# Kernel optimization log

Hardware: AMD Instinct MI355X
Metric: run time of the kernel (lower is better)

## Reference

```python
import jax, jax.numpy as jnp
import numpy as np

P = 16            # patch_size
D = 256           # hidden_dim == P*P (required by final reshape)
H = 8             # num_heads
HD = D // H       # head_dim


def _sinusoid(n, d):
    # standard sinusoidal positional encoding, interleaved sin/cos
    pos = jnp.arange(n, dtype=jnp.float32)[:, None]            # (n,1)
    i = jnp.arange(0, d, 2, dtype=jnp.float32)                 # (d/2,)
    div = jnp.exp(-i * (jnp.log(10000.0) / d))                 # (d/2,)
    ang = pos * div                                            # (n, d/2)
    return jnp.stack([jnp.sin(ang), jnp.cos(ang)], axis=-1).reshape(n, d)


def _patch_embed(x, w, b):
    # Conv2d(in_ch, D, kernel=P, stride=P) then flatten to (B, N, D)
    e = jax.lax.conv_general_dilated(
        x, w, window_strides=(P, P), padding='VALID',
        dimension_numbers=('NCHW', 'OIHW', 'NCHW'))
    e = e + b[None, :, None, None]
    B = e.shape[0]
    e = e.reshape(B, D, -1).transpose(0, 2, 1)                 # (B, N, D)
    e = e + _sinusoid(e.shape[1], D)[None]                     # positional enc
    return e.reshape(B, -1, H, HD).transpose(0, 2, 1, 3)       # (B, H, N, HD)


def setup_inputs() -> dict:
    key = jax.random.key(0)
    ks = jax.random.split(key, 12)
    B = 16
    inp = {
        'q': jax.random.normal(ks[0], (B, 3, 512, 512), jnp.float32),
        'k': jax.random.normal(ks[1], (B, 3, 512, 512), jnp.float32),
        'v': jax.random.normal(ks[2], (B, 3, 512, 512), jnp.float32),
        'a': jax.random.normal(ks[3], (B, 3, 256, 256), jnp.float32),
    }
    s = 0.02
    for idx, name in enumerate('qkva'):
        inp['w' + name] = jax.random.normal(ks[4 + 2 * idx], (D, 3, P, P), jnp.float32) * s
        inp['b' + name] = jnp.zeros((D,), jnp.float32)
    return inp


def reference(q, k, v, a, wq, bq, wk, bk, wv, bv, wa, ba):
    qh = _patch_embed(q, wq, bq)   # (B,H,Nq,HD), Nq=1024
    kh = _patch_embed(k, wk, bk)   # (B,H,Nk,HD)
    vh = _patch_embed(v, wv, bv)   # (B,H,Nk,HD)
    ah = _patch_embed(a, wa, ba)   # (B,H,Na,HD), Na=256
    scale = HD ** -0.5
    # agent attention: two small softmax matmuls then Q @ (K @ V)
    Qs = jax.nn.softmax(jnp.einsum('bhnd,bhmd->bhnm', qh, ah) * scale, axis=-1)  # (B,H,Nq,Na)
    Ks = jax.nn.softmax(jnp.einsum('bhmd,bhnd->bhmn', ah, kh) * scale, axis=-1)  # (B,H,Na,Nk)
    KV = jnp.einsum('bhmn,bhnd->bhmd', Ks, vh)                                   # (B,H,Na,HD)
    A = jnp.einsum('bhnm,bhmd->bhnd', Qs, KV)                                    # (B,H,Nq,HD)
    B = A.shape[0]
    attn = A.transpose(0, 2, 1, 3).reshape(B, -1, D)            # (B, Nq, D)
    N = attn.shape[1]
    g = int(N ** 0.5)                                           # grid side (32)
    HW = g * P                                                  # 512
    attn = attn.reshape(B, N, P, P)
    attn = attn.reshape(B, g, g, P, P).transpose(0, 1, 3, 2, 4).reshape(B, HW, HW)
    return attn
```

## Files before the change

kernel.cpp:

```cpp
#include <hip/hip_runtime.h>
#include <cstdint>
#include <cstddef>

typedef __bf16 bf16x8 __attribute__((ext_vector_type(8)));
typedef __bf16 bf16x4 __attribute__((ext_vector_type(4)));
typedef float f32x4 __attribute__((ext_vector_type(4)));
typedef unsigned short u16x4 __attribute__((ext_vector_type(4)));
typedef unsigned short u16x8 __attribute__((ext_vector_type(8)));

#define MFMA16(a, b, c) __builtin_amdgcn_mfma_f32_16x16x32_bf16(a, b, c, 0, 0, 0)

__device__ __forceinline__ unsigned short f2bf(float f) {
    unsigned u = __builtin_bit_cast(unsigned, f);
    u = (u + 0x7FFFu + ((u >> 16) & 1u)) >> 16;
    return (unsigned short)u;
}

__global__ __launch_bounds__(256)
void prep(float* __restrict__ pe, float* __restrict__ peT, unsigned short* __restrict__ Wb,
          const float* __restrict__ w0, const float* __restrict__ w1,
          const float* __restrict__ w2, const float* __restrict__ w3) {
    const int bx = blockIdx.x, t = threadIdx.x;
    const float LC = 0.03597789207808881f;
    if (bx < 1024) {
        int n = bx, d = t;
        float div = expf(-(float)(2 * (d >> 1)) * LC);
        float ang = (float)n * div;
        pe[n * 256 + d] = (d & 1) ? cosf(ang) : sinf(ang);
    } else if (bx < 1280) {
        int d = bx - 1024;
        float div = expf(-(float)(2 * (d >> 1)) * LC);
        f32x4 o;
        int n0 = t * 4;
#pragma unroll
        for (int e = 0; e < 4; ++e) {
            float ang = (float)(n0 + e) * div;
            o[e] = (d & 1) ? cosf(ang) : sinf(ang);
        }
        *(f32x4*)&peT[(size_t)d * 1024 + n0] = o;
    } else {
        int i = bx - 1280;
        int tensor = i / 192, blk = i - tensor * 192;
        const float* w = (tensor == 0) ? w0 : (tensor == 1) ? w1 : (tensor == 2) ? w2 : w3;
        int idx4 = blk * 256 + t;
        int d = idx4 / 192;
        int kq = (idx4 - d * 192) * 4;
        f32x4 v = *(const f32x4*)(w + (size_t)idx4 * 4);
        u16x4 o;
#pragma unroll
        for (int e = 0; e < 4; ++e) o[e] = f2bf(v[e]);
        unsigned short* dst = Wb + (size_t)tensor * 196608
                            + (d >> 4) * 12288 + (kq >> 5) * 512
                            + (d & 15) * 32 + (kq & 31);
        *(u16x4*)dst = o;
    }
}

struct EArgs {
    const float* src;
    const unsigned short* Wb;
    const float* bias;
    const float* pe;
    const float* peT;
    unsigned short* dst;
    int Np, lgNp, lgG, S, trans;
};

typedef unsigned short AsTile[128][40];

template<bool TR>
__device__ __forceinline__ void embed_body(const EArgs& A, int m0, int nh, AsTile* As) {
    const int t = threadIdx.x, lane = t & 63, wid = t >> 6;
    const int l15 = lane & 15, l4 = lane >> 4;
    const int wr = wid >> 1, wc = wid & 1;
    const int S = A.S;

    const int sp = t & 127;
    const int sh = t >> 7;
    {
    }
    int p_s = m0 + sp;
    int b_s = p_s >> A.lgNp, n_s = p_s & (A.Np - 1);
    int gy_s = n_s >> A.lgG, gx_s = n_s & ((1 << A.lgG) - 1);
    const float* sbase = A.src + ((size_t)(b_s * 3) * S + gy_s * 16 + sh) * (size_t)S + gx_s * 16;

    auto loadA = [&](int kt, f32x4* g) {
        const float* a = sbase + ((size_t)(kt >> 3) * S + ((kt & 7) << 1)) * (size_t)S;
        g[0] = *(const f32x4*)(a);
        g[1] = *(const f32x4*)(a + 4);
        g[2] = *(const f32x4*)(a + 8);
        g[3] = *(const f32x4*)(a + 12);
    };
    auto writeA = [&](int buf, const f32x4* g) {
        u16x8 o0, o1;
#pragma unroll
        for (int e = 0; e < 4; ++e) {
            o0[e] = f2bf(g[0][e]); o0[4 + e] = f2bf(g[1][e]);
            o1[e] = f2bf(g[2][e]); o1[4 + e] = f2bf(g[3][e]);
        }
        *(u16x8*)&As[buf][sp][sh * 16] = o0;
        *(u16x8*)&As[buf][sp][sh * 16 + 8] = o1;
    };

    const unsigned short* wbase = A.Wb + (size_t)(nh * 8 + wc * 4) * 12288 + l15 * 32 + l4 * 8;
    auto loadW = [&](int kt, bf16x8* wf) {
#pragma unroll
        for (int j = 0; j < 4; ++j) {
            u16x8 r = *(const u16x8*)(wbase + j * 12288 + kt * 512);
            wf[j] = __builtin_bit_cast(bf16x8, r);
        }
    };

    f32x4 acc[4][4];
#pragma unroll
    for (int i = 0; i < 4; ++i)
#pragma unroll
        for (int j = 0; j < 4; ++j) acc[i][j] = f32x4{0.f, 0.f, 0.f, 0.f};

    f32x4 gaA[4], gaB[4];
    bf16x8 wfc[4];
    loadA(0, gaA);
    writeA(0, gaA);
    loadA(1, gaA);
    loadW(0, wfc);
    __syncthreads();

#pragma unroll 2
    for (int kt = 0; kt < 24; ++kt) {
        const int c = kt & 1;
        const int kA = (kt + 2 < 24) ? kt + 2 : 23;
        const int kW = (kt + 1 < 24) ? kt + 1 : 23;
        loadA(kA, gaB);
        bf16x8 wfn[4];
        loadW(kW, wfn);

        bf16x8 pf[4];
#pragma unroll
        for (int i = 0; i < 4; ++i)
            pf[i] = *(const bf16x8*)&As[c][wr * 64 + i * 16 + l15][l4 * 8];

#pragma unroll
        for (int i = 0; i < 4; ++i)
#pragma unroll
            for (int j = 0; j < 4; ++j) {
                if (TR) acc[i][j] = MFMA16(pf[i], wfc[j], acc[i][j]);
                else    acc[i][j] = MFMA16(wfc[j], pf[i], acc[i][j]);
            }

        writeA(c ^ 1, gaA);
        __syncthreads();
#pragma unroll
        for (int j = 0; j < 4; ++j) { gaA[j] = gaB[j]; wfc[j] = wfn[j]; }
    }

    if (!TR) {
#pragma unroll
        for (int j = 0; j < 4; ++j) {
            int d0 = nh * 128 + wc * 64 + j * 16 + l4 * 4;
            int hh = d0 >> 5, hd = d0 & 31;
            f32x4 bs = *(const f32x4*)&A.bias[d0];
#pragma unroll
            for (int i = 0; i < 4; ++i) {
                int p = m0 + wr * 64 + i * 16 + l15;
                int b = p >> A.lgNp, n = p & (A.Np - 1);
                f32x4 pv = *(const f32x4*)&A.pe[n * 256 + d0];
                bf16x4 o;
#pragma unroll
                for (int r = 0; r < 4; ++r)
                    o[r] = (__bf16)(acc[i][j][r] + bs[r] + pv[r]);
                *(bf16x4*)&A.dst[(((size_t)(b * 8 + hh)) * A.Np + n) * 32 + hd] = o;
            }
        }
    } else {
#pragma unroll
        for (int j = 0; j < 4; ++j) {
            int d = nh * 128 + wc * 64 + j * 16 + l15;
            int hh = d >> 5, hd = d & 31;
            float bsv = A.bias[d];
#pragma unroll
            for (int i = 0; i < 4; ++i) {
                int p0 = m0 + wr * 64 + i * 16 + l4 * 4;
                int b = p0 >> A.lgNp, n0 = p0 & (A.Np - 1);
                f32x4 pv = *(const f32x4*)&A.peT[(size_t)d * 1024 + n0];
                bf16x4 o;
#pragma unroll
                for (int r = 0; r < 4; ++r)
                    o[r] = (__bf16)(acc[i][j][r] + bsv + pv[r]);
                *(bf16x4*)&A.dst[(((size_t)(b * 8 + hh)) * 32 + hd) * (size_t)A.Np + n0] = o;
            }
        }
    }
}

__global__ __launch_bounds__(256, 3)
void embed3(EArgs A0, EArgs A1, EArgs A2, EArgs A3) {
    __shared__ unsigned short As[2][128][40];
    const int bx = blockIdx.x;
    EArgs A; int lbx;
    if      (bx < 256) { A = A0; lbx = bx; }
    else if (bx < 512) { A = A1; lbx = bx - 256; }
    else if (bx < 768) { A = A2; lbx = bx - 512; }
    else               { A = A3; lbx = bx - 768; }
    const int m0 = (lbx >> 1) * 128;
    const int nh = lbx & 1;
    if (A.trans) embed_body<true>(A, m0, nh, As);
    else         embed_body<false>(A, m0, nh, As);
}

__global__ __launch_bounds__(512)
void s2kv_kernel(const unsigned short* __restrict__ ah_ws,
                 const unsigned short* __restrict__ kh_ws,
                 const unsigned short* __restrict__ vT_ws,
                 unsigned short* __restrict__ kvT_ws) {
    __shared__ unsigned short ahs[128][40];
    __shared__ unsigned short khs[128][40];
    __shared__ unsigned short vts[32][136];
    __shared__ unsigned short Ps[128][136];

    const int bid = blockIdx.x;
    const int half = bid & 1;
    const int h = (bid >> 1) & 7, b = bid >> 4;
    const int a0 = half * 128;
    const int t = threadIdx.x, lane = t & 63, wid = t >> 6;
    const int l15 = lane & 15, l4 = lane >> 4;
    const size_t bh = (size_t)(b * 8 + h);

    const unsigned short* ahp = ah_ws + (bh * 256 + a0) * 32;
    const unsigned short* khp = kh_ws + bh * 1024 * 32;
    const unsigned short* vtp = vT_ws + bh * 32 * 1024;

    {
        int row = t >> 2, kq = (t & 3) * 8;
        *(u16x8*)&ahs[row][kq] = *(const u16x8*)(ahp + row * 32 + kq);
    }
    __syncthreads();
    const bf16x8 af = *(const bf16x8*)&ahs[wid * 16 + l15][l4 * 8];

    const float scale = 0.17677669529663687f;
    float rs[4] = {0.f, 0.f, 0.f, 0.f};
    const f32x4 z = {0.f, 0.f, 0.f, 0.f};
    f32x4 kv[2];
    kv[0] = z; kv[1] = z;

    for (int kt = 0; kt < 8; ++kt) {
        const int n0 = kt * 128;
        __syncthreads();
        {
            int row = t >> 2, kq = (t & 3) * 8;
            *(u16x8*)&khs[row][kq] = *(const u16x8*)(khp + (size_t)(n0 + row) * 32 + kq);
        }
        {
            int row = t >> 4, cq = (t & 15) * 8;
            *(u16x8*)&vts[row][cq] = *(const u16x8*)(vtp + (size_t)row * 1024 + n0 + cq);
        }
        __syncthreads();
#pragma unroll
        for (int n16 = 0; n16 < 8; ++n16) {
            bf16x8 bfr = *(const bf16x8*)&khs[n16 * 16 + l15][l4 * 8];
            f32x4 s = MFMA16(af, bfr, z);
#pragma unroll
            for (int r = 0; r < 4; ++r) {
                float e = __expf(s[r] * scale);
                rs[r] += e;
                Ps[wid * 16 + l4 * 4 + r][n16 * 16 + l15] = f2bf(e);
            }
        }
        __syncthreads();
#pragma unroll
        for (int ks = 0; ks < 4; ++ks) {
            bf16x8 pa = *(const bf16x8*)&Ps[wid * 16 + l15][ks * 32 + l4 * 8];
#pragma unroll
            for (int n16 = 0; n16 < 2; ++n16) {
                bf16x8 vb = *(const bf16x8*)&vts[n16 * 16 + l15][ks * 32 + l4 * 8];
                kv[n16] = MFMA16(pa, vb, kv[n16]);
            }
        }
    }
#pragma unroll
    for (int r = 0; r < 4; ++r) {
        rs[r] += __shfl_xor(rs[r], 1, 64);
        rs[r] += __shfl_xor(rs[r], 2, 64);
        rs[r] += __shfl_xor(rs[r], 4, 64);
        rs[r] += __shfl_xor(rs[r], 8, 64);
    }
#pragma unroll
    for (int n16 = 0; n16 < 2; ++n16)
#pragma unroll
        for (int r = 0; r < 4; ++r) {
            int m = a0 + wid * 16 + l4 * 4 + r;
            int d = n16 * 16 + l15;
            kvT_ws[bh * 8192 + (size_t)d * 256 + m] = f2bf(kv[n16][r] / rs[r]);
        }
}

__global__ __launch_bounds__(256)
void qsa_kernel(const unsigned short* __restrict__ qh_ws,
                const unsigned short* __restrict__ ah_ws,
                const unsigned short* __restrict__ kvT_ws,
                float* __restrict__ out) {
    __shared__ unsigned short qhs[64][40];
    __shared__ unsigned short ahs[256][40];
    __shared__ unsigned short kvt[32][264];
    __shared__ unsigned short Ps[64][264];

    const int bid = blockIdx.x;
    const int qt = bid & 15, h = (bid >> 4) & 7, b = bid >> 7;
    const int m0 = qt * 64;
    const int t = threadIdx.x, lane = t & 63, wid = t >> 6;
    const int l15 = lane & 15, l4 = lane >> 4;
    const size_t bh = (size_t)(b * 8 + h);

    const unsigned short* qhp = qh_ws + (bh * 1024 + m0) * 32;
    const unsigned short* ahp = ah_ws + bh * 256 * 32;

    {
        int row = t >> 2, kq = (t & 3) * 8;
        *(u16x8*)&qhs[row][kq] = *(const u16x8*)(qhp + row * 32 + kq);
    }
    {
        *(u16x8*)&ahs[t][0]  = *(const u16x8*)(ahp + (size_t)t * 32);
        *(u16x8*)&ahs[t][8]  = *(const u16x8*)(ahp + (size_t)t * 32 + 8);
        *(u16x8*)&ahs[t][16] = *(const u16x8*)(ahp + (size_t)t * 32 + 16);
        *(u16x8*)&ahs[t][24] = *(const u16x8*)(ahp + (size_t)t * 32 + 24);
    }
#pragma unroll
    for (int i = 0; i < 4; ++i) {
        int chunk = t + i * 256;
        int row = chunk >> 5, cq = (chunk & 31) * 8;
        *(u16x8*)&kvt[row][cq] = *(const u16x8*)(kvT_ws + bh * 8192 + (size_t)row * 256 + cq);
    }
    __syncthreads();

    const bf16x8 qa = *(const bf16x8*)&qhs[wid * 16 + l15][l4 * 8];
    const float scale = 0.17677669529663687f;
    const f32x4 z = {0.f, 0.f, 0.f, 0.f};
    float rs[4] = {0.f, 0.f, 0.f, 0.f};
#pragma unroll
    for (int n16 = 0; n16 < 16; ++n16) {
        bf16x8 bfr = *(const bf16x8*)&ahs[n16 * 16 + l15][l4 * 8];
        f32x4 s = MFMA16(qa, bfr, z);
#pragma unroll
        for (int r = 0; r < 4; ++r) {
            float e = __expf(s[r] * scale);
            rs[r] += e;
            Ps[wid * 16 + l4 * 4 + r][n16 * 16 + l15] = f2bf(e);
        }
    }
#pragma unroll
    for (int r = 0; r < 4; ++r) {
        rs[r] += __shfl_xor(rs[r], 1, 64);
        rs[r] += __shfl_xor(rs[r], 2, 64);
        rs[r] += __shfl_xor(rs[r], 4, 64);
        rs[r] += __shfl_xor(rs[r], 8, 64);
    }
    __syncthreads();

    f32x4 o[2];
    o[0] = z; o[1] = z;
#pragma unroll
    for (int ks = 0; ks < 8; ++ks) {
        bf16x8 pa = *(const bf16x8*)&Ps[wid * 16 + l15][ks * 32 + l4 * 8];
#pragma unroll
        for (int n16 = 0; n16 < 2; ++n16) {
            bf16x8 kb = *(const bf16x8*)&kvt[n16 * 16 + l15][ks * 32 + l4 * 8];
            o[n16] = MFMA16(pa, kb, o[n16]);
        }
    }
#pragma unroll
    for (int n16 = 0; n16 < 2; ++n16) {
#pragma unroll
        for (int r = 0; r < 4; ++r) {
            int row = wid * 16 + l4 * 4 + r;
            int n = m0 + row;
            int gy = n >> 5, gx = n & 31;
            int hd = n16 * 16 + l15;
            int py = 2 * h + (hd >> 4), px = hd & 15;
            out[((size_t)b * 512 + gy * 16 + py) * 512 + gx * 16 + px] = o[n16][r] / rs[r];
        }
    }
}

extern "C" void kernel_launch(void* const* d_in, const int* in_sizes, int n_in,
                              void* d_out, int out_size, void* d_ws, size_t ws_size,
                              hipStream_t stream) {
    (void)in_sizes; (void)n_in; (void)out_size; (void)ws_size;

    const float* q  = (const float*)d_in[0];
    const float* k  = (const float*)d_in[1];
    const float* v  = (const float*)d_in[2];
    const float* a  = (const float*)d_in[3];
    const float* wq = (const float*)d_in[4];
    const float* bq = (const float*)d_in[5];
    const float* wk = (const float*)d_in[6];
    const float* bk = (const float*)d_in[7];
    const float* wv = (const float*)d_in[8];
    const float* bv = (const float*)d_in[9];
    const float* wa = (const float*)d_in[10];
    const float* ba = (const float*)d_in[11];
    float* out = (float*)d_out;

    char* ws = (char*)d_ws;
    float* pe           = (float*)(ws);
    float* peT          = (float*)(ws + 1048576);
    unsigned short* Wb  = (unsigned short*)(ws + 2097152);
    unsigned short* kvT = (unsigned short*)(ws);
    unsigned short* qh  = (unsigned short*)(ws + 3670016);
    unsigned short* kh  = (unsigned short*)(ws + 12058624);
    unsigned short* ah  = (unsigned short*)(ws + 20447232);
    unsigned short* vT  = (unsigned short*)(ws + 22544384);

    prep<<<2048, 256, 0, stream>>>(pe, peT, Wb, wq, wk, wv, wa);

    EArgs Aq = { q, Wb,              bq, pe, peT, qh, 1024, 10, 5, 512, 0 };
    EArgs Ak = { k, Wb + 196608,     bk, pe, peT, kh, 1024, 10, 5, 512, 0 };
    EArgs Av = { v, Wb + 2 * 196608, bv, pe, peT, vT, 1024, 10, 5, 512, 1 };
    EArgs Aa = { a, Wb + 3 * 196608, ba, pe, peT, ah,  256,  8, 4, 256, 0 };
    embed3<<<832, 256, 0, stream>>>(Aq, Ak, Av, Aa);

    s2kv_kernel<<<256, 512, 0, stream>>>(ah, kh, vT, kvT);
    qsa_kernel<<<2048, 256, 0, stream>>>(qh, ah, kvT, out);
}
```

Baseline: 117.1 us.

## Stage embed GEMM operands via direct global-to-LDS loads with swizzled layout

The patch-embed GEMM now loads fp32 image patches and bf16 weights straight from global memory into shared memory with global_load_lds, double-buffered and synchronised with explicit vmcnt waits and barriers. Previously A went through registers with fp32-to-bf16 conversion and W was loaded directly into registers. The bf16 conversion of A now happens after the shared-memory read, and both tiles use an XOR swizzle (the prep kernel reorders the weights to match) to avoid bank conflicts. Keeping A in fp32 doubles its shared-memory footprint, so the occupancy hint drops from 3 to 2 blocks.

```diff
diff --git a/kernel.cpp b/kernel.cpp
--- a/kernel.cpp
+++ b/kernel.cpp
@@ -9,6 +9,11 @@
 typedef unsigned short u16x8 __attribute__((ext_vector_type(8)));
 
 #define MFMA16(a, b, c) __builtin_amdgcn_mfma_f32_16x16x32_bf16(a, b, c, 0, 0, 0)
+
+#define GLOAD16(g, l)                                                          \
+    __builtin_amdgcn_global_load_lds(                                          \
+        (const __attribute__((address_space(1))) unsigned int*)(g),            \
+        (__attribute__((address_space(3))) unsigned int*)(l), 16, 0, 0)
 
 __device__ __forceinline__ unsigned short f2bf(float f) {
     unsigned u = __builtin_bit_cast(unsigned, f);
@@ -44,14 +49,16 @@
         const float* w = (tensor == 0) ? w0 : (tensor == 1) ? w1 : (tensor == 2) ? w2 : w3;
         int idx4 = blk * 256 + t;
         int d = idx4 / 192;
-        int kq = (idx4 - d * 192) * 4;
+        int kq4 = idx4 - d * 192;
         f32x4 v = *(const f32x4*)(w + (size_t)idx4 * 4);
         u16x4 o;
 #pragma unroll
         for (int e = 0; e < 4; ++e) o[e] = f2bf(v[e]);
+        int d16 = d & 15, kq_in = kq4 & 7;
+        int slot = (kq_in >> 1) ^ ((d16 >> 1) & 3);
         unsigned short* dst = Wb + (size_t)tensor * 196608
-                            + (d >> 4) * 12288 + (kq >> 5) * 512
-                            + (d & 15) * 32 + (kq & 31);
+                            + (d >> 4) * 12288 + (kq4 >> 3) * 512
+                            + d16 * 32 + slot * 8 + (kq_in & 1) * 4;
         *(u16x4*)dst = o;
     }
 }
@@ -66,92 +73,101 @@
     int Np, lgNp, lgG, S, trans;
 };
 
-typedef unsigned short AsTile[128][40];
-
 template<bool TR>
-__device__ __forceinline__ void embed_body(const EArgs& A, int m0, int nh, AsTile* As) {
+__device__ __forceinline__ void embed_body(const EArgs& A, int m0, int nh,
+                                           float* Abuf0, float* Abuf1,
+                                           unsigned short* Wbuf0, unsigned short* Wbuf1) {
     const int t = threadIdx.x, lane = t & 63, wid = t >> 6;
     const int l15 = lane & 15, l4 = lane >> 4;
     const int wr = wid >> 1, wc = wid & 1;
     const int S = A.S;
-
-    const int sp = t & 127;
-    const int sh = t >> 7;
-    {
-    }
-    int p_s = m0 + sp;
-    int b_s = p_s >> A.lgNp, n_s = p_s & (A.Np - 1);
-    int gy_s = n_s >> A.lgG, gx_s = n_s & ((1 << A.lgG) - 1);
-    const float* sbase = A.src + ((size_t)(b_s * 3) * S + gy_s * 16 + sh) * (size_t)S + gx_s * 16;
-
-    auto loadA = [&](int kt, f32x4* g) {
-        const float* a = sbase + ((size_t)(kt >> 3) * S + ((kt & 7) << 1)) * (size_t)S;
-        g[0] = *(const f32x4*)(a);
-        g[1] = *(const f32x4*)(a + 4);
-        g[2] = *(const f32x4*)(a + 8);
-        g[3] = *(const f32x4*)(a + 12);
+    const size_t S2 = (size_t)S * S;
+
+    float* Ab[2] = { Abuf0, Abuf1 };
+    unsigned short* Wbf[2] = { Wbuf0, Wbuf1 };
+
+    const int kqL = (lane & 7) ^ (lane >> 3);
+    const float* aP[4];
+#pragma unroll
+    for (int i = 0; i < 4; ++i) {
+        int p = (wid * 4 + i) * 8 + (lane >> 3);
+        int m = m0 + p;
+        int b = m >> A.lgNp, n = m & (A.Np - 1);
+        int gy = n >> A.lgG, gx = n & ((1 << A.lgG) - 1);
+        aP[i] = A.src + ((size_t)(b * 3) * S + gy * 16 + (kqL >> 2)) * (size_t)S
+              + gx * 16 + (kqL & 3) * 4;
+    }
+    const unsigned short* wP[2];
+#pragma unroll
+    for (int j = 0; j < 2; ++j)
+        wP[j] = A.Wb + (size_t)(nh * 8 + wid * 2 + j) * 12288 + lane * 8;
+
+    auto stage = [&](int kt, int buf) {
+        size_t aoff = (size_t)(kt >> 3) * S2 + (size_t)((kt & 7) * 2) * S;
+#pragma unroll
+        for (int i = 0; i < 4; ++i)
+            GLOAD16(aP[i] + aoff, Ab[buf] + (wid * 4 + i) * 256);
+#pragma unroll
+        for (int j = 0; j < 2; ++j)
+            GLOAD16(wP[j] + kt * 512, Wbf[buf] + (wid * 2 + j) * 512);
     };
-    auto writeA = [&](int buf, const f32x4* g) {
-        u16x8 o0, o1;
-#pragma unroll
-        for (int e = 0; e < 4; ++e) {
-            o0[e] = f2bf(g[0][e]); o0[4 + e] = f2bf(g[1][e]);
-            o1[e] = f2bf(g[2][e]); o1[4 + e] = f2bf(g[3][e]);
-        }
-        *(u16x8*)&As[buf][sp][sh * 16] = o0;
-        *(u16x8*)&As[buf][sp][sh * 16 + 8] = o1;
+
+    f32x4 acc[4][4];
+#pragma unroll
+    for (int i = 0; i < 4; ++i)
+#pragma unroll
+        for (int j = 0; j < 4; ++j) acc[i][j] = f32x4{0.f, 0.f, 0.f, 0.f};
+
+    auto compute = [&](int c) {
+        bf16x8 pf[4];
+#pragma unroll
+        for (int i = 0; i < 4; ++i) {
+            const char* base = (const char*)Ab[c] + (wr * 64 + i * 16 + l15) * 128;
+            f32x4 lo = *(const f32x4*)(base + (((2 * l4) ^ (l15 & 7)) << 4));
+            f32x4 hi = *(const f32x4*)(base + (((2 * l4 + 1) ^ (l15 & 7)) << 4));
+            bf16x8 v;
+#pragma unroll
+            for (int e = 0; e < 4; ++e) { v[e] = (__bf16)lo[e]; v[4 + e] = (__bf16)hi[e]; }
+            pf[i] = v;
+        }
+        bf16x8 wf[4];
+#pragma unroll
+        for (int j = 0; j < 4; ++j) {
+            const char* base = (const char*)Wbf[c] + (wc * 4 + j) * 1024;
+            u16x8 r = *(const u16x8*)(base + l15 * 64 + ((l4 ^ ((l15 >> 1) & 3)) << 4));
+            wf[j] = __builtin_bit_cast(bf16x8, r);
+        }
+#pragma unroll
+        for (int i = 0; i < 4; ++i)
+#pragma unroll
+            for (int j = 0; j < 4; ++j) {
+                if (TR) acc[i][j] = MFMA16(pf[i], wf[j], acc[i][j]);
+                else    acc[i][j] = MFMA16(wf[j], pf[i], acc[i][j]);
+            }
     };
 
-    const unsigned short* wbase = A.Wb + (size_t)(nh * 8 + wc * 4) * 12288 + l15 * 32 + l4 * 8;
-    auto loadW = [&](int kt, bf16x8* wf) {
-#pragma unroll
-        for (int j = 0; j < 4; ++j) {
-            u16x8 r = *(const u16x8*)(wbase + j * 12288 + kt * 512);
-            wf[j] = __builtin_bit_cast(bf16x8, r);
-        }
-    };
-
-    f32x4 acc[4][4];
-#pragma unroll
-    for (int i = 0; i < 4; ++i)
-#pragma unroll
-        for (int j = 0; j < 4; ++j) acc[i][j] = f32x4{0.f, 0.f, 0.f, 0.f};
-
-    f32x4 gaA[4], gaB[4];
-    bf16x8 wfc[4];
-    loadA(0, gaA);
-    writeA(0, gaA);
-    loadA(1, gaA);
-    loadW(0, wfc);
-    __syncthreads();
+    stage(0, 0);
+    stage(1, 1);
 
 #pragma unroll 2
-    for (int kt = 0; kt < 24; ++kt) {
-        const int c = kt & 1;
-        const int kA = (kt + 2 < 24) ? kt + 2 : 23;
-        const int kW = (kt + 1 < 24) ? kt + 1 : 23;
-        loadA(kA, gaB);
-        bf16x8 wfn[4];
-        loadW(kW, wfn);
-
-        bf16x8 pf[4];
-#pragma unroll
-        for (int i = 0; i < 4; ++i)
-            pf[i] = *(const bf16x8*)&As[c][wr * 64 + i * 16 + l15][l4 * 8];
-
-#pragma unroll
-        for (int i = 0; i < 4; ++i)
-#pragma unroll
-            for (int j = 0; j < 4; ++j) {
-                if (TR) acc[i][j] = MFMA16(pf[i], wfc[j], acc[i][j]);
-                else    acc[i][j] = MFMA16(wfc[j], pf[i], acc[i][j]);
-            }
-
-        writeA(c ^ 1, gaA);
-        __syncthreads();
-#pragma unroll
-        for (int j = 0; j < 4; ++j) { gaA[j] = gaB[j]; wfc[j] = wfn[j]; }
-    }
+    for (int kt = 0; kt < 22; ++kt) {
+        asm volatile("s_waitcnt vmcnt(6)" ::: "memory");
+        __builtin_amdgcn_s_barrier();
+        compute(kt & 1);
+        asm volatile("s_waitcnt lgkmcnt(0)" ::: "memory");
+        __builtin_amdgcn_sched_barrier(0);
+        __builtin_amdgcn_s_barrier();
+        stage(kt + 2, kt & 1);
+    }
+    asm volatile("s_waitcnt vmcnt(6)" ::: "memory");
+    __builtin_amdgcn_s_barrier();
+    compute(0);
+    asm volatile("s_waitcnt lgkmcnt(0)" ::: "memory");
+    __builtin_amdgcn_sched_barrier(0);
+    __builtin_amdgcn_s_barrier();
+    asm volatile("s_waitcnt vmcnt(0)" ::: "memory");
+    __builtin_amdgcn_s_barrier();
+    compute(1);
 
     if (!TR) {
 #pragma unroll
@@ -192,9 +208,10 @@
     }
 }
 
-__global__ __launch_bounds__(256, 3)
-void embed3(EArgs A0, EArgs A1, EArgs A2, EArgs A3) {
-    __shared__ unsigned short As[2][128][40];
+__global__ __launch_bounds__(256, 2)
+void embed4(EArgs A0, EArgs A1, EArgs A2, EArgs A3) {
+    __shared__ float Abuf[2][4096];
+    __shared__ unsigned short Wbuf[2][4096];
     const int bx = blockIdx.x;
     EArgs A; int lbx;
     if      (bx < 256) { A = A0; lbx = bx; }
@@ -203,8 +220,8 @@
     else               { A = A3; lbx = bx - 768; }
     const int m0 = (lbx >> 1) * 128;
     const int nh = lbx & 1;
-    if (A.trans) embed_body<true>(A, m0, nh, As);
-    else         embed_body<false>(A, m0, nh, As);
+    if (A.trans) embed_body<true>(A, m0, nh, Abuf[0], Abuf[1], Wbuf[0], Wbuf[1]);
+    else         embed_body<false>(A, m0, nh, Abuf[0], Abuf[1], Wbuf[0], Wbuf[1]);
 }
 
 __global__ __launch_bounds__(512)
@@ -415,7 +432,7 @@
     EArgs Ak = { k, Wb + 196608,     bk, pe, peT, kh, 1024, 10, 5, 512, 0 };
     EArgs Av = { v, Wb + 2 * 196608, bv, pe, peT, vT, 1024, 10, 5, 512, 1 };
     EArgs Aa = { a, Wb + 3 * 196608, ba, pe, peT, ah,  256,  8, 4, 256, 0 };
-    embed3<<<832, 256, 0, stream>>>(Aq, Ak, Av, Aa);
+    embed4<<<832, 256, 0, stream>>>(Aq, Ak, Av, Aa);
 
     s2kv_kernel<<<256, 512, 0, stream>>>(ah, kh, vT, kvT);
     qsa_kernel<<<2048, 256, 0, stream>>>(qh, ah, kvT, out);
```

New measurement: 117.5 us. About the same (+0.3%).

## Restructure patch-embed GEMM to per-wave full-N tiles without LDS staging

Applied to the files above, without the earlier changes.

The embedding GEMM kernel now gives each wave 32 patch rows and all 256 output channels, loading the input patches straight from global memory into registers. It converts them to bf16 in registers, using a 3-deep register prefetch, instead of staging through shared memory with block-wide barriers. This drops the LDS round trip and __syncthreads, and halves the grid from 832 to 416 blocks. The cost is a larger accumulator register footprint (32 f32x4 per lane), a lower occupancy target, and weights read from global/L2 by every wave rather than being shared across a block tile.

```diff
diff --git a/kernel.cpp b/kernel.cpp
--- a/kernel.cpp
+++ b/kernel.cpp
@@ -66,103 +66,97 @@
     int Np, lgNp, lgG, S, trans;
 };
 
-typedef unsigned short AsTile[128][40];
-
 template<bool TR>
-__device__ __forceinline__ void embed_body(const EArgs& A, int m0, int nh, AsTile* As) {
-    const int t = threadIdx.x, lane = t & 63, wid = t >> 6;
+__device__ __forceinline__ void embed_body(const EArgs& A, int m0) {
+    const int lane = threadIdx.x & 63;
     const int l15 = lane & 15, l4 = lane >> 4;
-    const int wr = wid >> 1, wc = wid & 1;
     const int S = A.S;
-
-    const int sp = t & 127;
-    const int sh = t >> 7;
-    {
-    }
-    int p_s = m0 + sp;
-    int b_s = p_s >> A.lgNp, n_s = p_s & (A.Np - 1);
-    int gy_s = n_s >> A.lgG, gx_s = n_s & ((1 << A.lgG) - 1);
-    const float* sbase = A.src + ((size_t)(b_s * 3) * S + gy_s * 16 + sh) * (size_t)S + gx_s * 16;
+    const size_t S2 = (size_t)S * S;
+
+    const float* pbase[2];
+    int nn[2], bb[2];
+#pragma unroll
+    for (int i = 0; i < 2; ++i) {
+        int p = m0 + i * 16 + l15;
+        int b = p >> A.lgNp, n = p & (A.Np - 1);
+        nn[i] = n; bb[i] = b;
+        int gy = n >> A.lgG, gx = n & ((1 << A.lgG) - 1);
+        pbase[i] = A.src + ((size_t)(b * 3) * S + gy * 16 + (l4 >> 1)) * (size_t)S
+                 + gx * 16 + (l4 & 1) * 8;
+    }
+    const unsigned short* wbase = A.Wb + l15 * 32 + l4 * 8;
+
+    f32x4 acc[2][16];
+#pragma unroll
+    for (int i = 0; i < 2; ++i)
+#pragma unroll
+        for (int j = 0; j < 16; ++j) acc[i][j] = f32x4{0.f, 0.f, 0.f, 0.f};
 
     auto loadA = [&](int kt, f32x4* g) {
-        const float* a = sbase + ((size_t)(kt >> 3) * S + ((kt & 7) << 1)) * (size_t)S;
-        g[0] = *(const f32x4*)(a);
-        g[1] = *(const f32x4*)(a + 4);
-        g[2] = *(const f32x4*)(a + 8);
-        g[3] = *(const f32x4*)(a + 12);
+        size_t aoff = (size_t)(kt >> 3) * S2 + (size_t)((kt & 7) * 2) * (size_t)S;
+        g[0] = *(const f32x4*)(pbase[0] + aoff);
+        g[1] = *(const f32x4*)(pbase[0] + aoff + 4);
+        g[2] = *(const f32x4*)(pbase[1] + aoff);
+        g[3] = *(const f32x4*)(pbase[1] + aoff + 4);
     };
-    auto writeA = [&](int buf, const f32x4* g) {
-        u16x8 o0, o1;
-#pragma unroll
-        for (int e = 0; e < 4; ++e) {
-            o0[e] = f2bf(g[0][e]); o0[4 + e] = f2bf(g[1][e]);
-            o1[e] = f2bf(g[2][e]); o1[4 + e] = f2bf(g[3][e]);
-        }
-        *(u16x8*)&As[buf][sp][sh * 16] = o0;
-        *(u16x8*)&As[buf][sp][sh * 16 + 8] = o1;
-    };
-
-    const unsigned short* wbase = A.Wb + (size_t)(nh * 8 + wc * 4) * 12288 + l15 * 32 + l4 * 8;
-    auto loadW = [&](int kt, bf16x8* wf) {
-#pragma unroll
-        for (int j = 0; j < 4; ++j) {
-            u16x8 r = *(const u16x8*)(wbase + j * 12288 + kt * 512);
+
+    f32x4 apf[3][4];
+    loadA(0, apf[0]);
+    loadA(1, apf[1]);
+    loadA(2, apf[2]);
+
+#pragma unroll 3
+    for (int kt = 0; kt < 24; ++kt) {
+        const int sl = kt % 3;
+        bf16x8 pf[2];
+#pragma unroll
+        for (int i = 0; i < 2; ++i) {
+            bf16x8 v;
+#pragma unroll
+            for (int e = 0; e < 4; ++e) {
+                v[e]     = (__bf16)apf[sl][2 * i][e];
+                v[4 + e] = (__bf16)apf[sl][2 * i + 1][e];
+            }
+            pf[i] = v;
+        }
+        if (kt < 21) loadA(kt + 3, apf[sl]);
+
+        bf16x8 wf[8];
+#pragma unroll
+        for (int j = 0; j < 8; ++j) {
+            u16x8 r = *(const u16x8*)(wbase + (size_t)j * 12288 + kt * 512);
             wf[j] = __builtin_bit_cast(bf16x8, r);
         }
-    };
-
-    f32x4 acc[4][4];
-#pragma unroll
-    for (int i = 0; i < 4; ++i)
-#pragma unroll
-        for (int j = 0; j < 4; ++j) acc[i][j] = f32x4{0.f, 0.f, 0.f, 0.f};
-
-    f32x4 gaA[4], gaB[4];
-    bf16x8 wfc[4];
-    loadA(0, gaA);
-    writeA(0, gaA);
-    loadA(1, gaA);
-    loadW(0, wfc);
-    __syncthreads();
-
-#pragma unroll 2
-    for (int kt = 0; kt < 24; ++kt) {
-        const int c = kt & 1;
-        const int kA = (kt + 2 < 24) ? kt + 2 : 23;
-        const int kW = (kt + 1 < 24) ? kt + 1 : 23;
-        loadA(kA, gaB);
-        bf16x8 wfn[4];
-        loadW(kW, wfn);
-
-        bf16x8 pf[4];
-#pragma unroll
-        for (int i = 0; i < 4; ++i)
-            pf[i] = *(const bf16x8*)&As[c][wr * 64 + i * 16 + l15][l4 * 8];
-
-#pragma unroll
-        for (int i = 0; i < 4; ++i)
-#pragma unroll
-            for (int j = 0; j < 4; ++j) {
-                if (TR) acc[i][j] = MFMA16(pf[i], wfc[j], acc[i][j]);
-                else    acc[i][j] = MFMA16(wfc[j], pf[i], acc[i][j]);
-            }
-
-        writeA(c ^ 1, gaA);
-        __syncthreads();
-#pragma unroll
-        for (int j = 0; j < 4; ++j) { gaA[j] = gaB[j]; wfc[j] = wfn[j]; }
+#pragma unroll
+        for (int j = 0; j < 8; ++j)
+#pragma unroll
+            for (int i = 0; i < 2; ++i) {
+                if (TR) acc[i][j] = MFMA16(pf[i], wf[j], acc[i][j]);
+                else    acc[i][j] = MFMA16(wf[j], pf[i], acc[i][j]);
+            }
+#pragma unroll
+        for (int j = 0; j < 8; ++j) {
+            u16x8 r = *(const u16x8*)(wbase + (size_t)(8 + j) * 12288 + kt * 512);
+            wf[j] = __builtin_bit_cast(bf16x8, r);
+        }
+#pragma unroll
+        for (int j = 0; j < 8; ++j)
+#pragma unroll
+            for (int i = 0; i < 2; ++i) {
+                if (TR) acc[i][8 + j] = MFMA16(pf[i], wf[j], acc[i][8 + j]);
+                else    acc[i][8 + j] = MFMA16(wf[j], pf[i], acc[i][8 + j]);
+            }
     }
 
     if (!TR) {
 #pragma unroll
-        for (int j = 0; j < 4; ++j) {
-            int d0 = nh * 128 + wc * 64 + j * 16 + l4 * 4;
+        for (int j = 0; j < 16; ++j) {
+            int d0 = j * 16 + l4 * 4;
             int hh = d0 >> 5, hd = d0 & 31;
             f32x4 bs = *(const f32x4*)&A.bias[d0];
 #pragma unroll
-            for (int i = 0; i < 4; ++i) {
-                int p = m0 + wr * 64 + i * 16 + l15;
-                int b = p >> A.lgNp, n = p & (A.Np - 1);
+            for (int i = 0; i < 2; ++i) {
+                int n = nn[i], b = bb[i];
                 f32x4 pv = *(const f32x4*)&A.pe[n * 256 + d0];
                 bf16x4 o;
 #pragma unroll
@@ -173,13 +167,13 @@
         }
     } else {
 #pragma unroll
-        for (int j = 0; j < 4; ++j) {
-            int d = nh * 128 + wc * 64 + j * 16 + l15;
+        for (int j = 0; j < 16; ++j) {
+            int d = j * 16 + l15;
             int hh = d >> 5, hd = d & 31;
             float bsv = A.bias[d];
 #pragma unroll
-            for (int i = 0; i < 4; ++i) {
-                int p0 = m0 + wr * 64 + i * 16 + l4 * 4;
+            for (int i = 0; i < 2; ++i) {
+                int p0 = m0 + i * 16 + l4 * 4;
                 int b = p0 >> A.lgNp, n0 = p0 & (A.Np - 1);
                 f32x4 pv = *(const f32x4*)&A.peT[(size_t)d * 1024 + n0];
                 bf16x4 o;
@@ -192,19 +186,17 @@
     }
 }
 
-__global__ __launch_bounds__(256, 3)
-void embed3(EArgs A0, EArgs A1, EArgs A2, EArgs A3) {
-    __shared__ unsigned short As[2][128][40];
+__global__ __launch_bounds__(256, 2)
+void embed6(EArgs A0, EArgs A1, EArgs A2, EArgs A3) {
     const int bx = blockIdx.x;
     EArgs A; int lbx;
-    if      (bx < 256) { A = A0; lbx = bx; }
-    else if (bx < 512) { A = A1; lbx = bx - 256; }
-    else if (bx < 768) { A = A2; lbx = bx - 512; }
-    else               { A = A3; lbx = bx - 768; }
-    const int m0 = (lbx >> 1) * 128;
-    const int nh = lbx & 1;
-    if (A.trans) embed_body<true>(A, m0, nh, As);
-    else         embed_body<false>(A, m0, nh, As);
+    if      (bx < 128) { A = A0; lbx = bx; }
+    else if (bx < 256) { A = A1; lbx = bx - 128; }
+    else if (bx < 384) { A = A2; lbx = bx - 256; }
+    else               { A = A3; lbx = bx - 384; }
+    const int m0 = lbx * 128 + (threadIdx.x >> 6) * 32;
+    if (A.trans) embed_body<true>(A, m0);
+    else         embed_body<false>(A, m0);
 }
 
 __global__ __launch_bounds__(512)
@@ -415,7 +407,7 @@
     EArgs Ak = { k, Wb + 196608,     bk, pe, peT, kh, 1024, 10, 5, 512, 0 };
     EArgs Av = { v, Wb + 2 * 196608, bv, pe, peT, vT, 1024, 10, 5, 512, 1 };
     EArgs Aa = { a, Wb + 3 * 196608, ba, pe, peT, ah,  256,  8, 4, 256, 0 };
-    embed3<<<832, 256, 0, stream>>>(Aq, Ak, Av, Aa);
+    embed6<<<416, 256, 0, stream>>>(Aq, Ak, Av, Aa);
 
     s2kv_kernel<<<256, 512, 0, stream>>>(ah, kh, vT, kvT);
     qsa_kernel<<<2048, 256, 0, stream>>>(qh, ah, kvT, out);
```

After: 140.2 us. 19.7% more time.
